# Optimization experiments

Measured on AMD Instinct MI355X. Metric: run time of the kernel, lower is better.

The kernel has to match this reference:

```python
import jax, jax.numpy as jnp
import numpy as np

K = 3  # kernel size per dim


def _conv3d(x, w, b):
    # x: (N,C,T,H,W), w: (O,C,3,3,3), stride 1, padding 1
    y = jax.lax.conv_general_dilated(
        x, w, window_strides=(1, 1, 1),
        padding=((1, 1), (1, 1), (1, 1)),
        dimension_numbers=('NCDHW', 'OIDHW', 'NCDHW'))
    return y + b[None, :, None, None, None]


def _dcn_hw(x, w_off, b_off, w, b):
    """DeformConvPack_d with dimension='HW': offsets only along H and W."""
    N, C, T, H, W = x.shape
    KK = K * K * K  # 27 taps
    # offset prediction conv: (N, 2*27, T, H, W) -> (N, 27, 2, T, H, W)
    off = _conv3d(x, w_off, b_off).reshape(N, KK, 2, T, H, W)
    kt, kh, kw = [a.reshape(-1) for a in jnp.meshgrid(
        jnp.arange(K), jnp.arange(K), jnp.arange(K), indexing='ij')]
    # temporal sampling positions are integer (no offset along T)
    p_t = jnp.arange(T)[None, :] + kt[:, None] - 1              # (27, T)
    t_ok = ((p_t >= 0) & (p_t < T))[None, :, :, None, None]     # (1,27,T,1,1)
    p_tc = jnp.clip(p_t, 0, T - 1)[None, :, :, None, None]
    # fractional spatial sampling positions: (N,27,T,H,W)
    p_h = (jnp.arange(H, dtype=x.dtype)[None, None, None, :, None]
           + (kh - 1).astype(x.dtype)[None, :, None, None, None] + off[:, :, 0])
    p_w = (jnp.arange(W, dtype=x.dtype)[None, None, None, None, :]
           + (kw - 1).astype(x.dtype)[None, :, None, None, None] + off[:, :, 1])
    h0f = jnp.floor(p_h); w0f = jnp.floor(p_w)
    lh = (p_h - h0f)[..., None]; lw = (p_w - w0f)[..., None]
    h0 = h0f.astype(jnp.int32); w0 = w0f.astype(jnp.int32)
    xt = jnp.transpose(x, (0, 2, 3, 4, 1))  # (N,T,H,W,C) for gather
    bidx = jnp.arange(N)[:, None, None, None, None]

    def corner(hi, wi):
        ok = t_ok & (hi >= 0) & (hi < H) & (wi >= 0) & (wi < W)
        v = xt[bidx, p_tc, jnp.clip(hi, 0, H - 1), jnp.clip(wi, 0, W - 1)]
        return jnp.where(ok[..., None], v, jnp.zeros((), x.dtype))

    # bilinear interpolation with zero padding outside bounds
    samp = ((1 - lh) * (1 - lw)) * corner(h0, w0) \
         + ((1 - lh) * lw) * corner(h0, w0 + 1) \
         + (lh * (1 - lw)) * corner(h0 + 1, w0) \
         + (lh * lw) * corner(h0 + 1, w0 + 1)     # (N,27,T,H,W,C)
    O = w.shape[0]
    out = jnp.einsum('nkthwc,ock->nothw', samp, w.reshape(O, C, KK))
    return out + b[None, :, None, None, None]


def setup_inputs() -> dict:
    key = jax.random.key(0)
    ks = jax.random.split(key, 6)
    N, C, T, H, W = 1, 64, 7, 48, 48
    fan = 1.0 / np.sqrt(C * 27)
    return {
        'x': jax.random.normal(ks[0], (N, C, T, H, W), jnp.float32),
        'w_off0': jax.random.normal(ks[1], (54, C, 3, 3, 3), jnp.float32) * 0.01,
        'b_off0': jnp.zeros((54,), jnp.float32),
        'w0': jax.random.normal(ks[2], (C, C, 3, 3, 3), jnp.float32) * fan,
        'b0': jnp.zeros((C,), jnp.float32),
        'w_off1': jax.random.normal(ks[3], (54, C, 3, 3, 3), jnp.float32) * 0.01,
        'b_off1': jnp.zeros((54,), jnp.float32),
        'w1': jax.random.normal(ks[4], (C, C, 3, 3, 3), jnp.float32) * fan,
        'b1': jnp.zeros((C,), jnp.float32),
    }


def reference(x, w_off0, b_off0, w0, b0, w_off1, b_off1, w1, b1):
    h = _dcn_hw(x, w_off0, b_off0, w0, b0)
    h = jnp.where(h >= 0, h, 0.1 * h)  # LeakyReLU(0.1)
    return _dcn_hw(h, w_off1, b_off1, w1, b1) + x
```

## Files before the change

kernel.cpp:

```cpp
#include <hip/hip_runtime.h>

#define T_ 7
#define H_ 48
#define W_ 48
#define P_ 16128
#define HW_ 2304

typedef __attribute__((ext_vector_type(8))) short short8;
typedef __attribute__((ext_vector_type(4))) float f32x4;
typedef __attribute__((ext_vector_type(4))) unsigned u32x4;

__device__ __forceinline__ unsigned short f2bf(float f) {
  union { float f; unsigned u; } x{f};
  unsigned r = x.u + 0x7FFFu + ((x.u >> 16) & 1u);
  return (unsigned short)(r >> 16);
}
__device__ __forceinline__ float blo(unsigned u) {
  union { unsigned u; float f; } x{u << 16};
  return x.f;
}
__device__ __forceinline__ float bhi(unsigned u) {
  union { unsigned u; float f; } x{u & 0xFFFF0000u};
  return x.f;
}
__device__ __forceinline__ unsigned pack2(float a, float b) {
  return (unsigned)f2bf(a) | ((unsigned)f2bf(b) << 16);
}
__device__ __forceinline__ int xcd_swz(int bid, int nwg) {
  int cpx = nwg >> 3;
  return (bid & 7) * cpx + (bid >> 3);
}

struct Wgt { short8 b00, b01, b10, b11, b20, b21, b30, b31; };

__device__ __forceinline__ Wgt load_w(const unsigned short* base, int k, int lane) {
  const unsigned short* wp = base + (size_t)k * 4096 + lane * 8;
  Wgt w;
  w.b00 = *(const short8*)(wp);
  w.b01 = *(const short8*)(wp + 512);
  w.b10 = *(const short8*)(wp + 1024);
  w.b11 = *(const short8*)(wp + 1536);
  w.b20 = *(const short8*)(wp + 2048);
  w.b21 = *(const short8*)(wp + 2560);
  w.b30 = *(const short8*)(wp + 3072);
  w.b31 = *(const short8*)(wp + 3584);
  return w;
}

__device__ __forceinline__ void mfma8(const Wgt& W, short8 af0, short8 af1,
                                      f32x4& c0, f32x4& c1, f32x4& c2, f32x4& c3) {
  c0 = __builtin_amdgcn_mfma_f32_16x16x32_bf16(af0, W.b00, c0, 0, 0, 0);
  c0 = __builtin_amdgcn_mfma_f32_16x16x32_bf16(af1, W.b01, c0, 0, 0, 0);
  c1 = __builtin_amdgcn_mfma_f32_16x16x32_bf16(af0, W.b10, c1, 0, 0, 0);
  c1 = __builtin_amdgcn_mfma_f32_16x16x32_bf16(af1, W.b11, c1, 0, 0, 0);
  c2 = __builtin_amdgcn_mfma_f32_16x16x32_bf16(af0, W.b20, c2, 0, 0, 0);
  c2 = __builtin_amdgcn_mfma_f32_16x16x32_bf16(af1, W.b21, c2, 0, 0, 0);
  c3 = __builtin_amdgcn_mfma_f32_16x16x32_bf16(af0, W.b30, c3, 0, 0, 0);
  c3 = __builtin_amdgcn_mfma_f32_16x16x32_bf16(af1, W.b31, c3, 0, 0, 0);
}

__global__ void k_prep_x(const float* __restrict__ in, unsigned short* __restrict__ outb) {
  __shared__ float tile[64][65];
  int p0 = blockIdx.x * 64;
  int l = threadIdx.x & 63;
  int g = threadIdx.x >> 6;
#pragma unroll
  for (int i = 0; i < 16; ++i) {
    int c = g * 16 + i;
    tile[c][l] = in[c * P_ + p0 + l];
  }
  __syncthreads();
#pragma unroll
  for (int i = 0; i < 16; ++i) {
    int p = g * 16 + i;
    outb[(p0 + p) * 64 + l] = f2bf(tile[l][p]);
  }
}

__global__ void k_prep_w4(const float* __restrict__ s0, const float* __restrict__ s1,
                          const float* __restrict__ s2, const float* __restrict__ s3,
                          unsigned short* __restrict__ d0, unsigned short* __restrict__ d1,
                          unsigned short* __restrict__ d2, unsigned short* __restrict__ d3) {
  int y = blockIdx.y;
  const float* w = (y == 0) ? s0 : (y == 1) ? s1 : (y == 2) ? s2 : s3;
  unsigned short* wt = (y == 0) ? d0 : (y == 1) ? d1 : (y == 2) ? d2 : d3;
  int OC = (y < 2) ? 54 : 64;
  int idx = blockIdx.x * 256 + threadIdx.x;
  int j = idx & 7;
  int l = (idx >> 3) & 63;
  int kc = (idx >> 9) & 1;
  int nt = (idx >> 10) & 3;
  int k = idx >> 12;
  int o = nt * 16 + (l & 15);
  int c = kc * 32 + (l >> 4) * 8 + j;
  wt[idx] = (o < OC) ? f2bf(w[(o * 64 + c) * 27 + k]) : (unsigned short)0;
}

__global__ __launch_bounds__(256) void k_off4w(const unsigned short* __restrict__ xclb,
                                               const unsigned short* __restrict__ wAs,
                                               const float* __restrict__ boff,
                                               float* __restrict__ offt2) {
  __shared__ f32x4 red[4][4][64];
  int p0 = xcd_swz(blockIdx.x, gridDim.x) * 32;
  int t = p0 / HW_;
  int r0 = p0 - t * HW_;
  int h0r = r0 / W_;
  int w0s = r0 - h0r * W_;
  int h1r = h0r + (w0s == 32 ? 1 : 0);
  int w1s = (w0s == 32) ? 0 : w0s + 16;
  int tid = threadIdx.x;
  int lane = tid & 63, wid = tid >> 6;
  int pt = lane & 15, grp = lane >> 4;

  f32x4 zacc{0.f, 0.f, 0.f, 0.f};
  f32x4 aA0 = zacc, aA1 = zacc, aA2 = zacc, aA3 = zacc;
  f32x4 aB0 = zacc, aB1 = zacc, aB2 = zacc, aB3 = zacc;
  const short8 zero8{0, 0, 0, 0, 0, 0, 0, 0};
  int kbeg = wid * 7;

#pragma unroll
  for (int kk = 0; kk < 7; ++kk) {
    int kraw = kbeg + kk;
    int k = min(kraw, 26);
    int kt = k / 9;
    int r9 = k - kt * 9;
    int kh = r9 / 3;
    int kw = r9 - (r9 / 3) * 3;
    int t2 = t + kt - 1;
    bool tok = (kraw < 27) & ((unsigned)t2 < (unsigned)T_);
    int t2c = min(max(t2, 0), T_ - 1);

    Wgt W = load_w(wAs, k, lane);
    {
      int h2 = h0r + kh - 1;
      int w2 = w0s + pt + kw - 1;
      bool ok = tok & ((unsigned)h2 < (unsigned)H_) & ((unsigned)w2 < (unsigned)W_);
      int h2c = min(max(h2, 0), H_ - 1);
      int w2c = min(max(w2, 0), W_ - 1);
      const unsigned short* ap = xclb + ((size_t)(t2c * HW_ + h2c * W_ + w2c) * 64 + grp * 8);
      short8 a0 = *(const short8*)ap;
      short8 a1 = *(const short8*)(ap + 32);
      a0 = ok ? a0 : zero8;
      a1 = ok ? a1 : zero8;
      mfma8(W, a0, a1, aA0, aA1, aA2, aA3);
    }
    {
      int h2 = h1r + kh - 1;
      int w2 = w1s + pt + kw - 1;
      bool ok = tok & ((unsigned)h2 < (unsigned)H_) & ((unsigned)w2 < (unsigned)W_);
      int h2c = min(max(h2, 0), H_ - 1);
      int w2c = min(max(w2, 0), W_ - 1);
      const unsigned short* ap = xclb + ((size_t)(t2c * HW_ + h2c * W_ + w2c) * 64 + grp * 8);
      short8 a0 = *(const short8*)ap;
      short8 a1 = *(const short8*)(ap + 32);
      a0 = ok ? a0 : zero8;
      a1 = ok ? a1 : zero8;
      mfma8(W, a0, a1, aB0, aB1, aB2, aB3);
    }
  }

  int oc = wid * 16 + pt;
  float bb = (oc < 54) ? boff[oc] : 0.f;
  int kidx = oc >> 1, d = oc & 1;

  red[wid][0][lane] = aA0;
  red[wid][1][lane] = aA1;
  red[wid][2][lane] = aA2;
  red[wid][3][lane] = aA3;
  __syncthreads();
  {
    f32x4 s = red[0][wid][lane];
    s = s + red[1][wid][lane];
    s = s + red[2][wid][lane];
    s = s + red[3][wid][lane];
    if (oc < 54) {
#pragma unroll
      for (int r = 0; r < 4; ++r) {
        int p = p0 + grp * 4 + r;
        offt2[((size_t)kidx * P_ + p) * 2 + d] = s[r] + bb;
      }
    }
  }
  __syncthreads();
  red[wid][0][lane] = aB0;
  red[wid][1][lane] = aB1;
  red[wid][2][lane] = aB2;
  red[wid][3][lane] = aB3;
  __syncthreads();
  {
    f32x4 s = red[0][wid][lane];
    s = s + red[1][wid][lane];
    s = s + red[2][wid][lane];
    s = s + red[3][wid][lane];
    if (oc < 54) {
#pragma unroll
      for (int r = 0; r < 4; ++r) {
        int p = p0 + 16 + grp * 4 + r;
        offt2[((size_t)kidx * P_ + p) * 2 + d] = s[r] + bb;
      }
    }
  }
}

template <int MODE>
__global__ __launch_bounds__(256) void k_samp16(
    const unsigned short* __restrict__ xclb, const float* __restrict__ offt2,
    const unsigned short* __restrict__ wBs, const float* __restrict__ bias,
    const float* __restrict__ resid, float* __restrict__ out32,
    unsigned short* __restrict__ outb) {
  __shared__ union LDSu {
    struct {
      u32x4 raw[4][16][2][16];
      int abuf[4][16][2];
      unsigned short sA[4][16][72];
    } lp;
    f32x4 red[4][4][64];
  } lds;
  int p0 = xcd_swz(blockIdx.x, gridDim.x) * 16;
  int t = p0 / HW_;
  int r0 = p0 - t * HW_;
  int h_r = r0 / W_;
  int w_s = r0 - h_r * W_;
  int tid = threadIdx.x;
  int lane = tid & 63, wid = tid >> 6;
  int pt = lane & 15, grp = lane >> 4;
  int lq = lane >> 4;
  int ck16 = lane & 15;

  f32x4 zacc{0.f, 0.f, 0.f, 0.f};
  f32x4 a0c = zacc, a1c = zacc, a2c = zacc, a3c = zacc;
  int kbeg = wid * 7;

#pragma clang loop unroll(disable)
  for (int kk = 0; kk < 7; ++kk) {
    int kraw = kbeg + kk;
    int k = min(kraw, 26);
    int kt = k / 9;
    int r9 = k - kt * 9;
    int kh = r9 / 3;
    int kw = r9 - (r9 / 3) * 3;
    int t2 = t + kt - 1;
    bool tok = (kraw < 27) & ((unsigned)t2 < (unsigned)T_);
    int t2c = min(max(t2, 0), T_ - 1);

    Wgt W = load_w(wBs, k, lane);

    float2 o2 = *(const float2*)(offt2 + ((size_t)k * P_ + p0 + pt) * 2);
    float ph = (float)(h_r + kh - 1) + o2.x;
    float pw = (float)(w_s + pt + kw - 1) + o2.y;
    float hf = floorf(ph), wf = floorf(pw);
    float lh = ph - hf, lw = pw - wf;
    int h0 = (int)hf, w0i = (int)wf;
    int h1 = h0 + 1, w1 = w0i + 1;
    bool h0ok = ((unsigned)h0 < (unsigned)H_), h1ok = ((unsigned)h1 < (unsigned)H_);
    bool w0ok = ((unsigned)w0i < (unsigned)W_), w1ok = ((unsigned)w1 < (unsigned)W_);
    int h0c = min(max(h0, 0), H_ - 1), h1c = min(max(h1, 0), H_ - 1);
    int w0c = min(max(w0i, 0), W_ - 1), w1c = min(max(w1, 0), W_ - 1);
    float omlh = 1.f - lh, omlw = 1.f - lw;
    float g00 = (tok & h0ok & w0ok) ? omlh * omlw : 0.f;
    float g01 = (tok & h0ok & w1ok) ? omlh * lw : 0.f;
    float g10 = (tok & h1ok & w0ok) ? lh * omlw : 0.f;
    float g11 = (tok & h1ok & w1ok) ? lh * lw : 0.f;

    int ws = min(max(w0i, 0), W_ - 2);
    int sel0 = w0c - ws;
    int sel1 = w1c - ws;
    if (grp == 0) {
      lds.lp.abuf[wid][pt][0] = (t2c * HW_ + h0c * W_ + ws) * 64;
      lds.lp.abuf[wid][pt][1] = (t2c * HW_ + h1c * W_ + ws) * 64;
    }
    __builtin_amdgcn_wave_barrier();

    u32x4 gb0, gb1, gb2, gb3, gb4, gb5, gb6, gb7;
    {
      int pl0 = lq, pl1 = 4 + lq, pl2 = 8 + lq, pl3 = 12 + lq;
      const unsigned short* c0p = xclb + (size_t)lds.lp.abuf[wid][pl0][0] + ck16 * 8;
      const unsigned short* c1p = xclb + (size_t)lds.lp.abuf[wid][pl0][1] + ck16 * 8;
      const unsigned short* c2p = xclb + (size_t)lds.lp.abuf[wid][pl1][0] + ck16 * 8;
      const unsigned short* c3p = xclb + (size_t)lds.lp.abuf[wid][pl1][1] + ck16 * 8;
      const unsigned short* c4p = xclb + (size_t)lds.lp.abuf[wid][pl2][0] + ck16 * 8;
      const unsigned short* c5p = xclb + (size_t)lds.lp.abuf[wid][pl2][1] + ck16 * 8;
      const unsigned short* c6p = xclb + (size_t)lds.lp.abuf[wid][pl3][0] + ck16 * 8;
      const unsigned short* c7p = xclb + (size_t)lds.lp.abuf[wid][pl3][1] + ck16 * 8;
      gb0 = *(const u32x4*)c0p;
      gb1 = *(const u32x4*)c1p;
      gb2 = *(const u32x4*)c2p;
      gb3 = *(const u32x4*)c3p;
      gb4 = *(const u32x4*)c4p;
      gb5 = *(const u32x4*)c5p;
      gb6 = *(const u32x4*)c6p;
      gb7 = *(const u32x4*)c7p;
    }
    __builtin_amdgcn_wave_barrier();
    {
      int pl0 = lq, pl1 = 4 + lq, pl2 = 8 + lq, pl3 = 12 + lq;
      lds.lp.raw[wid][pl0][0][ck16 ^ pl0] = gb0;
      lds.lp.raw[wid][pl0][1][ck16 ^ pl0] = gb1;
      lds.lp.raw[wid][pl1][0][ck16 ^ pl1] = gb2;
      lds.lp.raw[wid][pl1][1][ck16 ^ pl1] = gb3;
      lds.lp.raw[wid][pl2][0][ck16 ^ pl2] = gb4;
      lds.lp.raw[wid][pl2][1][ck16 ^ pl2] = gb5;
      lds.lp.raw[wid][pl3][0][ck16 ^ pl3] = gb6;
      lds.lp.raw[wid][pl3][1][ck16 ^ pl3] = gb7;
    }
    __builtin_amdgcn_wave_barrier();

    int b0 = sel0 * 8 + 2 * grp;
    int b1 = sel1 * 8 + 2 * grp;
    u32x4 A0 = lds.lp.raw[wid][pt][0][(b0) ^ pt];
    u32x4 A1 = lds.lp.raw[wid][pt][0][(b0 + 1) ^ pt];
    u32x4 B0 = lds.lp.raw[wid][pt][0][(b1) ^ pt];
    u32x4 B1 = lds.lp.raw[wid][pt][0][(b1 + 1) ^ pt];
    u32x4 C0 = lds.lp.raw[wid][pt][1][(b0) ^ pt];
    u32x4 C1 = lds.lp.raw[wid][pt][1][(b0 + 1) ^ pt];
    u32x4 D0 = lds.lp.raw[wid][pt][1][(b1) ^ pt];
    u32x4 D1 = lds.lp.raw[wid][pt][1][(b1 + 1) ^ pt];
    __builtin_amdgcn_wave_barrier();

#define LERPU(a, b, c, d)                                                   \
  pack2(g00 * blo(a) + g01 * blo(b) + g10 * blo(c) + g11 * blo(d),          \
        g00 * bhi(a) + g01 * bhi(b) + g10 * bhi(c) + g11 * bhi(d))
    u32x4 v0, v1;
    v0[0] = LERPU(A0[0], B0[0], C0[0], D0[0]);
    v0[1] = LERPU(A0[1], B0[1], C0[1], D0[1]);
    v0[2] = LERPU(A0[2], B0[2], C0[2], D0[2]);
    v0[3] = LERPU(A0[3], B0[3], C0[3], D0[3]);
    v1[0] = LERPU(A1[0], B1[0], C1[0], D1[0]);
    v1[1] = LERPU(A1[1], B1[1], C1[1], D1[1]);
    v1[2] = LERPU(A1[2], B1[2], C1[2], D1[2]);
    v1[3] = LERPU(A1[3], B1[3], C1[3], D1[3]);
#undef LERPU

    __builtin_amdgcn_wave_barrier();
    *(u32x4*)&lds.lp.sA[wid][pt][grp * 16] = v0;
    *(u32x4*)&lds.lp.sA[wid][pt][grp * 16 + 8] = v1;
    __builtin_amdgcn_wave_barrier();
    short8 af0 = *(const short8*)&lds.lp.sA[wid][pt][grp * 8];
    short8 af1 = *(const short8*)&lds.lp.sA[wid][pt][32 + grp * 8];
    __builtin_amdgcn_wave_barrier();

    mfma8(W, af0, af1, a0c, a1c, a2c, a3c);
  }

  int ch = wid * 16 + pt;
  float bb = bias[ch];

  __syncthreads();
  lds.red[wid][0][lane] = a0c;
  lds.red[wid][1][lane] = a1c;
  lds.red[wid][2][lane] = a2c;
  lds.red[wid][3][lane] = a3c;
  __syncthreads();
  {
    f32x4 s = lds.red[0][wid][lane];
    s = s + lds.red[1][wid][lane];
    s = s + lds.red[2][wid][lane];
    s = s + lds.red[3][wid][lane];
#pragma unroll
    for (int r = 0; r < 4; ++r) {
      int p = p0 + grp * 4 + r;
      float v = s[r] + bb;
      if (MODE == 0) {
        v = (v >= 0.f) ? v : 0.1f * v;
        outb[(size_t)p * 64 + ch] = f2bf(v);
      } else {
        out32[(size_t)ch * P_ + p] = v + resid[(size_t)ch * P_ + p];
      }
    }
  }
}

extern "C" void kernel_launch(void* const* d_in, const int* in_sizes, int n_in,
                              void* d_out, int out_size, void* d_ws, size_t ws_size,
                              hipStream_t stream) {
  const float* x      = (const float*)d_in[0];
  const float* w_off0 = (const float*)d_in[1];
  const float* b_off0 = (const float*)d_in[2];
  const float* w0     = (const float*)d_in[3];
  const float* b0     = (const float*)d_in[4];
  const float* w_off1 = (const float*)d_in[5];
  const float* b_off1 = (const float*)d_in[6];
  const float* w1     = (const float*)d_in[7];
  const float* b1     = (const float*)d_in[8];
  float* out = (float*)d_out;

  char* base = (char*)d_ws;
  unsigned short* x_clb = (unsigned short*)base;
  unsigned short* h_clb = (unsigned short*)(base + 2064384);
  float*          offt2 = (float*)(base + 4128768);
  unsigned short* wA0   = (unsigned short*)(base + 7612416);
  unsigned short* wA1   = (unsigned short*)(base + 7833600);
  unsigned short* wB0   = (unsigned short*)(base + 8054784);
  unsigned short* wB1   = (unsigned short*)(base + 8275968);

  hipLaunchKernelGGL(k_prep_x, dim3(252), dim3(256), 0, stream, x, x_clb);
  hipLaunchKernelGGL(k_prep_w4, dim3(432, 4), dim3(256), 0, stream,
                     w_off0, w_off1, w0, w1, wA0, wA1, wB0, wB1);

  hipLaunchKernelGGL(k_off4w, dim3(504), dim3(256), 0, stream, x_clb, wA0, b_off0, offt2);
  hipLaunchKernelGGL((k_samp16<0>), dim3(1008), dim3(256), 0, stream,
                     x_clb, offt2, wB0, b0, (const float*)nullptr, (float*)nullptr, h_clb);

  hipLaunchKernelGGL(k_off4w, dim3(504), dim3(256), 0, stream, h_clb, wA1, b_off1, offt2);
  hipLaunchKernelGGL((k_samp16<1>), dim3(1008), dim3(256), 0, stream,
                     h_clb, offt2, wB1, b1, x, out, (unsigned short*)nullptr);
}
```

Before: 84.02 us.

## Precompute bilinear sampling addresses and weights in a separate kernel

Adds a k_prec kernel that turns the offset field into per-(tap, pixel) gather base addresses, column selectors and masked bilinear weights, stored as 32 bytes per entry. The sampling kernel loads these records instead of recomputing floor/clamp/weight math. It also replaces the LDS address broadcast with wave shuffles, and zeroes the MFMA A operand for padded taps instead of folding that into the weights. The cost is two extra launches and roughly 14 MB extra global traffic per layer (27 × 16128 × 32 B written, then read back).

```diff
diff --git a/kernel.cpp b/kernel.cpp
--- a/kernel.cpp
+++ b/kernel.cpp
@@ -202,25 +202,69 @@
   }
 }
 
+__global__ __launch_bounds__(256) void k_prec(const float* __restrict__ offt2,
+                                              unsigned* __restrict__ pc) {
+  int idx = blockIdx.x * 256 + threadIdx.x;
+  int k = idx / P_;
+  int p = idx - k * P_;
+  int t = p / HW_;
+  int rr = p - t * HW_;
+  int h_p = rr / W_;
+  int w_p = rr - h_p * W_;
+  int kt = k / 9;
+  int r9 = k - kt * 9;
+  int kh = r9 / 3;
+  int kw = r9 - (r9 / 3) * 3;
+  int t2 = t + kt - 1;
+  bool tok = (unsigned)t2 < (unsigned)T_;
+  int t2c = min(max(t2, 0), T_ - 1);
+
+  float2 o2 = *(const float2*)(offt2 + (size_t)idx * 2);
+  float ph = (float)(h_p + kh - 1) + o2.x;
+  float pw = (float)(w_p + kw - 1) + o2.y;
+  float hf = floorf(ph), wf = floorf(pw);
+  float lh = ph - hf, lw = pw - wf;
+  int h0 = (int)hf, w0i = (int)wf;
+  int h1 = h0 + 1, w1 = w0i + 1;
+  bool h0ok = ((unsigned)h0 < (unsigned)H_), h1ok = ((unsigned)h1 < (unsigned)H_);
+  bool w0ok = ((unsigned)w0i < (unsigned)W_), w1ok = ((unsigned)w1 < (unsigned)W_);
+  int h0c = min(max(h0, 0), H_ - 1), h1c = min(max(h1, 0), H_ - 1);
+  int w0c = min(max(w0i, 0), W_ - 1), w1c = min(max(w1, 0), W_ - 1);
+  float omlh = 1.f - lh, omlw = 1.f - lw;
+  float g00 = (tok & h0ok & w0ok) ? omlh * omlw : 0.f;
+  float g01 = (tok & h0ok & w1ok) ? omlh * lw : 0.f;
+  float g10 = (tok & h1ok & w0ok) ? lh * omlw : 0.f;
+  float g11 = (tok & h1ok & w1ok) ? lh * lw : 0.f;
+
+  int ws = min(max(w0i, 0), W_ - 2);
+  u32x4 A, B;
+  A[0] = (unsigned)((t2c * HW_ + h0c * W_ + ws) * 64);
+  A[1] = (unsigned)((t2c * HW_ + h1c * W_ + ws) * 64);
+  A[2] = (unsigned)(w0c - ws);
+  A[3] = (unsigned)(w1c - ws);
+  B[0] = __builtin_bit_cast(unsigned, g00);
+  B[1] = __builtin_bit_cast(unsigned, g01);
+  B[2] = __builtin_bit_cast(unsigned, g10);
+  B[3] = __builtin_bit_cast(unsigned, g11);
+  u32x4* dst = (u32x4*)(pc + (size_t)idx * 8);
+  dst[0] = A;
+  dst[1] = B;
+}
+
 template <int MODE>
 __global__ __launch_bounds__(256) void k_samp16(
-    const unsigned short* __restrict__ xclb, const float* __restrict__ offt2,
+    const unsigned short* __restrict__ xclb, const unsigned* __restrict__ pc,
     const unsigned short* __restrict__ wBs, const float* __restrict__ bias,
     const float* __restrict__ resid, float* __restrict__ out32,
     unsigned short* __restrict__ outb) {
   __shared__ union LDSu {
     struct {
       u32x4 raw[4][16][2][16];
-      int abuf[4][16][2];
       unsigned short sA[4][16][72];
     } lp;
     f32x4 red[4][4][64];
   } lds;
   int p0 = xcd_swz(blockIdx.x, gridDim.x) * 16;
-  int t = p0 / HW_;
-  int r0 = p0 - t * HW_;
-  int h_r = r0 / W_;
-  int w_s = r0 - h_r * W_;
   int tid = threadIdx.x;
   int lane = tid & 63, wid = tid >> 6;
   int pt = lane & 15, grp = lane >> 4;
@@ -229,68 +273,40 @@
 
   f32x4 zacc{0.f, 0.f, 0.f, 0.f};
   f32x4 a0c = zacc, a1c = zacc, a2c = zacc, a3c = zacc;
+  const short8 zero8{0, 0, 0, 0, 0, 0, 0, 0};
   int kbeg = wid * 7;
 
 #pragma clang loop unroll(disable)
   for (int kk = 0; kk < 7; ++kk) {
     int kraw = kbeg + kk;
     int k = min(kraw, 26);
-    int kt = k / 9;
-    int r9 = k - kt * 9;
-    int kh = r9 / 3;
-    int kw = r9 - (r9 / 3) * 3;
-    int t2 = t + kt - 1;
-    bool tok = (kraw < 27) & ((unsigned)t2 < (unsigned)T_);
-    int t2c = min(max(t2, 0), T_ - 1);
+    bool okk = (kraw < 27);
 
     Wgt W = load_w(wBs, k, lane);
 
-    float2 o2 = *(const float2*)(offt2 + ((size_t)k * P_ + p0 + pt) * 2);
-    float ph = (float)(h_r + kh - 1) + o2.x;
-    float pw = (float)(w_s + pt + kw - 1) + o2.y;
-    float hf = floorf(ph), wf = floorf(pw);
-    float lh = ph - hf, lw = pw - wf;
-    int h0 = (int)hf, w0i = (int)wf;
-    int h1 = h0 + 1, w1 = w0i + 1;
-    bool h0ok = ((unsigned)h0 < (unsigned)H_), h1ok = ((unsigned)h1 < (unsigned)H_);
-    bool w0ok = ((unsigned)w0i < (unsigned)W_), w1ok = ((unsigned)w1 < (unsigned)W_);
-    int h0c = min(max(h0, 0), H_ - 1), h1c = min(max(h1, 0), H_ - 1);
-    int w0c = min(max(w0i, 0), W_ - 1), w1c = min(max(w1, 0), W_ - 1);
-    float omlh = 1.f - lh, omlw = 1.f - lw;
-    float g00 = (tok & h0ok & w0ok) ? omlh * omlw : 0.f;
-    float g01 = (tok & h0ok & w1ok) ? omlh * lw : 0.f;
-    float g10 = (tok & h1ok & w0ok) ? lh * omlw : 0.f;
-    float g11 = (tok & h1ok & w1ok) ? lh * lw : 0.f;
-
-    int ws = min(max(w0i, 0), W_ - 2);
-    int sel0 = w0c - ws;
-    int sel1 = w1c - ws;
-    if (grp == 0) {
-      lds.lp.abuf[wid][pt][0] = (t2c * HW_ + h0c * W_ + ws) * 64;
-      lds.lp.abuf[wid][pt][1] = (t2c * HW_ + h1c * W_ + ws) * 64;
-    }
-    __builtin_amdgcn_wave_barrier();
-
-    u32x4 gb0, gb1, gb2, gb3, gb4, gb5, gb6, gb7;
-    {
-      int pl0 = lq, pl1 = 4 + lq, pl2 = 8 + lq, pl3 = 12 + lq;
-      const unsigned short* c0p = xclb + (size_t)lds.lp.abuf[wid][pl0][0] + ck16 * 8;
-      const unsigned short* c1p = xclb + (size_t)lds.lp.abuf[wid][pl0][1] + ck16 * 8;
-      const unsigned short* c2p = xclb + (size_t)lds.lp.abuf[wid][pl1][0] + ck16 * 8;
-      const unsigned short* c3p = xclb + (size_t)lds.lp.abuf[wid][pl1][1] + ck16 * 8;
-      const unsigned short* c4p = xclb + (size_t)lds.lp.abuf[wid][pl2][0] + ck16 * 8;
-      const unsigned short* c5p = xclb + (size_t)lds.lp.abuf[wid][pl2][1] + ck16 * 8;
-      const unsigned short* c6p = xclb + (size_t)lds.lp.abuf[wid][pl3][0] + ck16 * 8;
-      const unsigned short* c7p = xclb + (size_t)lds.lp.abuf[wid][pl3][1] + ck16 * 8;
-      gb0 = *(const u32x4*)c0p;
-      gb1 = *(const u32x4*)c1p;
-      gb2 = *(const u32x4*)c2p;
-      gb3 = *(const u32x4*)c3p;
-      gb4 = *(const u32x4*)c4p;
-      gb5 = *(const u32x4*)c5p;
-      gb6 = *(const u32x4*)c6p;
-      gb7 = *(const u32x4*)c7p;
-    }
+    const unsigned* pcp = pc + ((size_t)k * P_ + p0 + pt) * 8;
+    u32x4 pcA = *(const u32x4*)pcp;
+    f32x4 pcB = *(const f32x4*)(pcp + 4);
+    int sel0 = (int)pcA[2], sel1 = (int)pcA[3];
+    float g00 = pcB[0], g01 = pcB[1], g10 = pcB[2], g11 = pcB[3];
+
+    int s0_0 = __shfl((int)pcA[0], lq);
+    int s1_0 = __shfl((int)pcA[1], lq);
+    int s0_1 = __shfl((int)pcA[0], 4 + lq);
+    int s1_1 = __shfl((int)pcA[1], 4 + lq);
+    int s0_2 = __shfl((int)pcA[0], 8 + lq);
+    int s1_2 = __shfl((int)pcA[1], 8 + lq);
+    int s0_3 = __shfl((int)pcA[0], 12 + lq);
+    int s1_3 = __shfl((int)pcA[1], 12 + lq);
+
+    u32x4 gb0 = *(const u32x4*)(xclb + (size_t)s0_0 + ck16 * 8);
+    u32x4 gb1 = *(const u32x4*)(xclb + (size_t)s1_0 + ck16 * 8);
+    u32x4 gb2 = *(const u32x4*)(xclb + (size_t)s0_1 + ck16 * 8);
+    u32x4 gb3 = *(const u32x4*)(xclb + (size_t)s1_1 + ck16 * 8);
+    u32x4 gb4 = *(const u32x4*)(xclb + (size_t)s0_2 + ck16 * 8);
+    u32x4 gb5 = *(const u32x4*)(xclb + (size_t)s1_2 + ck16 * 8);
+    u32x4 gb6 = *(const u32x4*)(xclb + (size_t)s0_3 + ck16 * 8);
+    u32x4 gb7 = *(const u32x4*)(xclb + (size_t)s1_3 + ck16 * 8);
     __builtin_amdgcn_wave_barrier();
     {
       int pl0 = lq, pl1 = 4 + lq, pl2 = 8 + lq, pl3 = 12 + lq;
@@ -339,6 +355,8 @@
     short8 af1 = *(const short8*)&lds.lp.sA[wid][pt][32 + grp * 8];
     __builtin_amdgcn_wave_barrier();
 
+    af0 = okk ? af0 : zero8;
+    af1 = okk ? af1 : zero8;
     mfma8(W, af0, af1, a0c, a1c, a2c, a3c);
   }
 
@@ -392,16 +410,19 @@
   unsigned short* wA1   = (unsigned short*)(base + 7833600);
   unsigned short* wB0   = (unsigned short*)(base + 8054784);
   unsigned short* wB1   = (unsigned short*)(base + 8275968);
+  unsigned*       pcb   = (unsigned*)(base + 8497152);
 
   hipLaunchKernelGGL(k_prep_x, dim3(252), dim3(256), 0, stream, x, x_clb);
   hipLaunchKernelGGL(k_prep_w4, dim3(432, 4), dim3(256), 0, stream,
                      w_off0, w_off1, w0, w1, wA0, wA1, wB0, wB1);
 
   hipLaunchKernelGGL(k_off4w, dim3(504), dim3(256), 0, stream, x_clb, wA0, b_off0, offt2);
+  hipLaunchKernelGGL(k_prec, dim3(1701), dim3(256), 0, stream, offt2, pcb);
   hipLaunchKernelGGL((k_samp16<0>), dim3(1008), dim3(256), 0, stream,
-                     x_clb, offt2, wB0, b0, (const float*)nullptr, (float*)nullptr, h_clb);
+                     x_clb, pcb, wB0, b0, (const float*)nullptr, (float*)nullptr, h_clb);
 
   hipLaunchKernelGGL(k_off4w, dim3(504), dim3(256), 0, stream, h_clb, wA1, b_off1, offt2);
+  hipLaunchKernelGGL(k_prec, dim3(1701), dim3(256), 0, stream, offt2, pcb);
   hipLaunchKernelGGL((k_samp16<1>), dim3(1008), dim3(256), 0, stream,
-                     h_clb, offt2, wB1, b1, x, out, (unsigned short*)nullptr);
-}
+                     h_clb, pcb, wB1, b1, x, out, (unsigned short*)nullptr);
+}
```

Measured after the change: 103.1 us. 22.7% more time.
